# Kernel tuning notes

Measured on AMD Instinct MI355X. Metric: run time of the kernel, lower is better.

## Reference

```python
import jax, jax.numpy as jnp
import numpy as np

B, Z, OUT, NODES = 2048, 64, 512, 64
TRIPLES = 3 * (NODES - 1)  # (self, left, right) per real node
EPS_BN = 1e-5
EPS_TLN = 1e-5
SLOPE = 0.01  # LeakyReLU default


def setup_inputs() -> dict:
    key = jax.random.key(0)
    ks = jax.random.split(key, 12)
    def n(k, shape, s=0.05):
        return jax.random.normal(k, shape, jnp.float32) * s
    inp = {
        "trees": jax.random.normal(ks[0], (B, Z), jnp.float32),
        "indexes": jax.random.randint(ks[1], (B, TRIPLES, 1), 0, NODES),
        # MLP: Linear(Z,64) -> BN -> Linear(64,256) -> BN -> Linear(256,1024) -> BN -> Linear(1024,4096) -> BN
        "w1": n(ks[2], (64, Z)),      "b1": jnp.zeros((64,), jnp.float32),
        "g1": jnp.ones((64,), jnp.float32),   "be1": jnp.zeros((64,), jnp.float32),
        "w2": n(ks[3], (256, 64)),    "b2": jnp.zeros((256,), jnp.float32),
        "g2": jnp.ones((256,), jnp.float32),  "be2": jnp.zeros((256,), jnp.float32),
        "w3": n(ks[4], (1024, 256)),  "b3": jnp.zeros((1024,), jnp.float32),
        "g3": jnp.ones((1024,), jnp.float32), "be3": jnp.zeros((1024,), jnp.float32),
        "w4": n(ks[5], (4096, 1024)), "b4": jnp.zeros((4096,), jnp.float32),
        "g4": jnp.ones((4096,), jnp.float32), "be4": jnp.zeros((4096,), jnp.float32),
        # BinaryTreeConv weights: Conv1d(in,out,kernel=3,stride=3) -> (out,in,3)
        "cw1": n(ks[6], (128, 64, 3)),  "cb1": jnp.zeros((128,), jnp.float32),
        "cw2": n(ks[7], (256, 128, 3)), "cb2": jnp.zeros((256,), jnp.float32),
        "cw3": n(ks[8], (OUT, 256, 3)), "cb3": jnp.zeros((OUT,), jnp.float32),
    }
    return inp


def _bn(x, g, b):
    # BatchNorm1d in training mode: batch statistics, biased variance
    m = jnp.mean(x, axis=0)
    v = jnp.var(x, axis=0)
    return g * (x - m) * jax.lax.rsqrt(v + EPS_BN) + b


def _lrelu(x):
    return jnp.where(x > 0, x, SLOPE * x)


def _tree_conv(x, idx, w, b):
    # x: (B, C, N); idx: (B, 3M) node indices; w: (O, C, 3)
    Bn, C, _ = x.shape
    expanded = jnp.take_along_axis(x, idx[:, None, :], axis=2)  # (B, C, 3M) gather
    expanded = expanded.reshape(Bn, C, -1, 3)                    # (B, C, M, 3)
    out = jnp.einsum('bcmk,ock->bom', expanded, w) + b[None, :, None]
    zero = jnp.zeros((Bn, w.shape[0], 1), x.dtype)               # re-attach null-node slot
    return jnp.concatenate([zero, out], axis=2)                  # (B, O, M+1)


def _tree_norm(x):
    # TreeLayerNorm: normalize over (channels, nodes) per sample; torch.std is unbiased
    m = jnp.mean(x, axis=(1, 2), keepdims=True)
    s = jnp.std(x, axis=(1, 2), ddof=1, keepdims=True)
    return (x - m) / (s + EPS_TLN)


def reference(trees, indexes, w1, b1, g1, be1, w2, b2, g2, be2, w3, b3, g3, be3,
              w4, b4, g4, be4, cw1, cb1, cw2, cb2, cw3, cb3):
    idx = indexes[..., 0]  # (B, 3M)
    h = _lrelu(_bn(trees @ w1.T + b1, g1, be1))
    h = _lrelu(_bn(h @ w2.T + b2, g2, be2))
    h = _lrelu(_bn(h @ w3.T + b3, g3, be3))
    h = _lrelu(_bn(h @ w4.T + b4, g4, be4))
    x = h.reshape(h.shape[0], 64, 64)  # (B, C=64, N=64)
    x = _lrelu(_tree_norm(_tree_conv(x, idx, cw1, cb1)))
    x = _lrelu(_tree_norm(_tree_conv(x, idx, cw2, cb2)))
    x = _lrelu(_tree_norm(_tree_conv(x, idx, cw3, cb3)))
    return x  # (B, OUT, 64)
```

## Files before the change

kernel.cpp:

```cpp
#include <hip/hip_runtime.h>

typedef unsigned short u16;
typedef unsigned int   u32;
typedef __attribute__((ext_vector_type(8))) short short8;
typedef __attribute__((ext_vector_type(4))) float f32x4;
typedef __attribute__((ext_vector_type(4))) u16  u16x4;

#define DI __device__ __forceinline__

DI float b2f(u16 v){ return __builtin_bit_cast(float, (u32)v << 16); }
DI u16 f2b(float f){ u32 u = __builtin_bit_cast(u32, f); return (u16)((u + 0x7fffu + ((u >> 16) & 1u)) >> 16); }
DI float lrelu(float v){ return v > 0.f ? v : 0.01f * v; }

__global__ __launch_bounds__(256)
void cvt_bf16(const float* __restrict__ in, u16* __restrict__ out, int n4)
{
  int i = blockIdx.x*256 + threadIdx.x;
  if (i >= n4) return;
  float4 v = ((const float4*)in)[i];
  u16x4 o; o[0]=f2b(v.x); o[1]=f2b(v.y); o[2]=f2b(v.z); o[3]=f2b(v.w);
  *(u16x4*)(out + (size_t)i*4) = o;
}

template<int BM, int BN, int WROWS, int WCOLS, int RT, int CT>
__global__ __launch_bounds__(WROWS*WCOLS*64)
void gemm_nt(const u16* __restrict__ A, const u16* __restrict__ W,
             float* __restrict__ Y, int M, int N, int K)
{
  constexpr int NT  = WROWS*WCOLS*64;
  constexpr int ALD = (BM*4)/NT;
  constexpr int BLD = (BN*4)/NT;
  __shared__ __align__(16) u16 As[BM*32];
  __shared__ __align__(16) u16 Bs[BN*32];
  const int tid  = threadIdx.x;
  const int wave = tid >> 6, lane = tid & 63;
  const int wr = wave / WCOLS, wc = wave % WCOLS;
  const int lrow = lane & 15, kg = lane >> 4;
  const int m0 = blockIdx.x * BM, n0 = blockIdx.y * BN;
  f32x4 acc[RT][CT] = {};
  for (int k0 = 0; k0 < K; k0 += 32) {
    uint4 av[ALD], bv[BLD];
#pragma unroll
    for (int i = 0; i < ALD; i++){ int x = tid + i*NT; av[i] = *(const uint4*)(A + (size_t)(m0 + (x>>2))*K + k0 + (x&3)*8); }
#pragma unroll
    for (int i = 0; i < BLD; i++){ int x = tid + i*NT; bv[i] = *(const uint4*)(W + (size_t)(n0 + (x>>2))*K + k0 + (x&3)*8); }
    __syncthreads();
#pragma unroll
    for (int i = 0; i < ALD; i++){ *(uint4*)(As + (tid + i*NT)*8) = av[i]; }
#pragma unroll
    for (int i = 0; i < BLD; i++){ *(uint4*)(Bs + (tid + i*NT)*8) = bv[i]; }
    __syncthreads();
    short8 af[RT], bfr[CT];
#pragma unroll
    for (int r = 0; r < RT; r++) af[r]  = *(const short8*)(As + ((wr*RT + r)*16 + lrow)*32 + kg*8);
#pragma unroll
    for (int c = 0; c < CT; c++) bfr[c] = *(const short8*)(Bs + ((wc*CT + c)*16 + lrow)*32 + kg*8);
#pragma unroll
    for (int r = 0; r < RT; r++)
#pragma unroll
      for (int c = 0; c < CT; c++)
        acc[r][c] = __builtin_amdgcn_mfma_f32_16x16x32_bf16(af[r], bfr[c], acc[r][c], 0, 0, 0);
  }
#pragma unroll
  for (int r = 0; r < RT; r++)
#pragma unroll
    for (int c = 0; c < CT; c++)
#pragma unroll
      for (int i = 0; i < 4; i++){
        int m = m0 + (wr*RT + r)*16 + kg*4 + i;
        int n = n0 + (wc*CT + c)*16 + lrow;
        Y[(size_t)m*N + n] = acc[r][c][i];
      }
}

__global__ __launch_bounds__(256)
void bn_partial(const float* __restrict__ Y, float* __restrict__ part, int N, int rowsPer)
{
  const int tx = threadIdx.x & 63, ty = threadIdx.x >> 6;
  const int n  = blockIdx.x*64 + tx;
  const int m0 = blockIdx.y * rowsPer;
  float s = 0.f, s2 = 0.f;
  for (int m = m0 + ty; m < m0 + rowsPer; m += 4){ float v = Y[(size_t)m*N + n]; s += v; s2 += v*v; }
  __shared__ float ls[4][64], ls2[4][64];
  ls[ty][tx] = s; ls2[ty][tx] = s2;
  __syncthreads();
  if (ty == 0){
    s  = ls[0][tx]+ls[1][tx]+ls[2][tx]+ls[3][tx];
    s2 = ls2[0][tx]+ls2[1][tx]+ls2[2][tx]+ls2[3][tx];
    part[(size_t)(blockIdx.y*2+0)*N + n] = s;
    part[(size_t)(blockIdx.y*2+1)*N + n] = s2;
  }
}

__global__ __launch_bounds__(256)
void bn_finalize(const float* __restrict__ part, const float* __restrict__ g,
                 const float* __restrict__ be, float* __restrict__ ss, int N, int M, int split)
{
  int n = blockIdx.x*256 + threadIdx.x;
  if (n >= N) return;
  float s = 0.f, s2 = 0.f;
  for (int i = 0; i < split; i++){ s += part[(size_t)(i*2+0)*N + n]; s2 += part[(size_t)(i*2+1)*N + n]; }
  float inv  = 1.f / (float)M;
  float mean = s * inv;
  float var  = fmaxf(s2*inv - mean*mean, 0.f);
  float sc   = g[n] * rsqrtf(var + 1e-5f);
  ss[n]     = sc;
  ss[N + n] = be[n] - mean*sc;
}

__global__ __launch_bounds__(256)
void bn_apply(const float* __restrict__ Y, const float* __restrict__ ss,
              u16* __restrict__ H, int total4, int N)
{
  int i = blockIdx.x*256 + threadIdx.x;
  if (i >= total4) return;
  float4 v = ((const float4*)Y)[i];
  int nb = (i*4) & (N-1);
  u16x4 o;
  o[0] = f2b(lrelu(v.x*ss[nb+0] + ss[N+nb+0]));
  o[1] = f2b(lrelu(v.y*ss[nb+1] + ss[N+nb+1]));
  o[2] = f2b(lrelu(v.z*ss[nb+2] + ss[N+nb+2]));
  o[3] = f2b(lrelu(v.w*ss[nb+3] + ss[N+nb+3]));
  *(u16x4*)(H + (size_t)i*4) = o;
}

__global__ __launch_bounds__(256)
void bn_apply4_t(const float* __restrict__ Y, const float* __restrict__ ss, u16* __restrict__ Xt)
{
  const int b = blockIdx.x, tid = threadIdx.x;
  __shared__ u16 t[64*65];
  for (int j = tid; j < 4096; j += 256){
    float v = Y[(size_t)b*4096 + j];
    v = lrelu(v*ss[j] + ss[4096 + j]);
    int c = j >> 6, n = j & 63;
    t[c*65 + n] = f2b(v);
  }
  __syncthreads();
  for (int e = tid; e < 4096; e += 256){
    int n = e >> 6, c = e & 63;
    Xt[(size_t)b*4096 + n*64 + c] = t[c*65 + n];
  }
}

__global__ __launch_bounds__(256)
void repack_w_frag(const float* __restrict__ w, u16* __restrict__ wr, int O, int C, int lgC)
{
  int e = blockIdx.x*256 + threadIdx.x;
  int R = 3*C;
  if (e >= O*R) return;
  int NK   = R >> 5;
  int j    = e & 7;
  int lane = (e >> 3) & 63;
  int blk  = e >> 9;
  int tr   = blk / NK, kb = blk - tr*NK;
  int row  = tr*16 + (lane & 15);
  int kcol = kb*32 + (lane >> 4)*8 + j;
  int k = kcol >> lgC; int c = kcol & (C-1);
  wr[e] = f2b(w[(size_t)row*R + c*3 + k]);
}

template<int C, int O, int WAVES, int MINW, bool PIPE, bool LAST>
__global__ __launch_bounds__(WAVES*64, MINW)
void conv_norm(const u16* __restrict__ Xin, const u16* __restrict__ Wr,
               const float* __restrict__ cb, const int* __restrict__ gidx,
               u16* __restrict__ Xout, float* __restrict__ Outf)
{
  constexpr int R    = 3*C;
  constexpr int NK   = R/32;
  constexpr int CSI  = C + 8;
  constexpr int RT   = O/(WAVES*16);
  constexpr int NT   = WAVES*64;
  constexpr int LGC  = (C==64)?6:((C==128)?7:8);
  constexpr int LG32 = LGC - 5;
  __shared__ __align__(16) u16 xs[65*CSI];
  __shared__ int idxs[192];
  __shared__ float red[2*WAVES];
  const int b = blockIdx.x, tid = threadIdx.x;
  const int wave = tid >> 6, lane = tid & 63;
  const int lrow = lane & 15, kg = lane >> 4;

  const u16* xg = Xin + (size_t)b*64*C;
  for (int e = tid; e < 64*(C/8); e += NT){
    int row = e/(C/8), t = e%(C/8);
    *(uint4*)(xs + row*CSI + t*8) = *(const uint4*)(xg + row*C + t*8);
  }
  for (int e = tid; e < C/8; e += NT){ uint4 z = {0,0,0,0}; *(uint4*)(xs + 64*CSI + e*8) = z; }
  if (tid < 189){ int v = gidx[b*189 + tid]; idxs[tid] = v & 63; }
  __syncthreads();

  int jr0[4], jr1[4], jr2[4];
#pragma unroll
  for (int ct = 0; ct < 4; ct++){
    int n = ct*16 + lrow;
    jr0[ct] = (n == 0) ? 64 : idxs[3*(n-1) + 0];
    jr1[ct] = (n == 0) ? 64 : idxs[3*(n-1) + 1];
    jr2[ct] = (n == 0) ? 64 : idxs[3*(n-1) + 2];
  }

  const u16* wbase = Wr + ((size_t)wave*NK << 9) + lane*8;

  auto loadA = [&](short8* af, int kb32){
#pragma unroll
    for (int r = 0; r < RT; r++)
      af[r] = *(const short8*)(wbase + (((size_t)(WAVES*r)*NK + kb32) << 9));
  };
  auto loadB = [&](short8* bfr, int kb32){
    const int k  = kb32 >> LG32;
    const int c0 = ((kb32*32) & (C-1)) + kg*8;
#pragma unroll
    for (int ct = 0; ct < 4; ct++){
      int row = (k == 0) ? jr0[ct] : ((k == 1) ? jr1[ct] : jr2[ct]);
      bfr[ct] = *(const short8*)(xs + row*CSI + c0);
    }
  };

  f32x4 acc[RT][4] = {};
  auto domfma = [&](short8* af, short8* bfr){
    __builtin_amdgcn_s_setprio(1);
#pragma unroll
    for (int r = 0; r < RT; r++)
#pragma unroll
      for (int ct = 0; ct < 4; ct++)
        acc[r][ct] = __builtin_amdgcn_mfma_f32_16x16x32_bf16(af[r], bfr[ct], acc[r][ct], 0, 0, 0);
    __builtin_amdgcn_s_setprio(0);
  };

  if constexpr (PIPE) {
    short8 afA[RT], bfA[4], afB[RT], bfB[4];
    loadA(afA, 0); loadB(bfA, 0);
    for (int kb32 = 0; kb32 < NK; kb32 += 2){
      loadA(afB, kb32+1); loadB(bfB, kb32+1);
      domfma(afA, bfA);
      if (kb32 + 2 < NK){ loadA(afA, kb32+2); loadB(bfA, kb32+2); }
      domfma(afB, bfB);
    }
  } else {
    for (int kb32 = 0; kb32 < NK; kb32++){
      short8 af[RT], bfr[4];
      loadA(af, kb32); loadB(bfr, kb32);
      domfma(af, bfr);
    }
  }

  float s = 0.f, s2 = 0.f;
#pragma unroll
  for (int r = 0; r < RT; r++)
#pragma unroll
    for (int i = 0; i < 4; i++){
      int o = (wave + WAVES*r)*16 + kg*4 + i;
      float bias = cb[o];
#pragma unroll
      for (int ct = 0; ct < 4; ct++){
        int n = ct*16 + lrow;
        float v = acc[r][ct][i];
        if (n != 0) v += bias;
        acc[r][ct][i] = v;
        s += v; s2 += v*v;
      }
    }
#pragma unroll
  for (int off = 32; off > 0; off >>= 1){ s += __shfl_down(s, off); s2 += __shfl_down(s2, off); }
  if (lane == 0){ red[wave] = s; red[WAVES + wave] = s2; }
  __syncthreads();
  if (tid == 0){
    float S = 0.f, S2 = 0.f;
    for (int w = 0; w < WAVES; w++){ S += red[w]; S2 += red[WAVES + w]; }
    const float NV = (float)(O*64);
    float mean = S / NV;
    float var  = fmaxf(S2/NV - mean*mean, 0.f) * (NV/(NV-1.f));
    float sc   = 1.f / (sqrtf(var) + 1e-5f);
    red[0] = mean; red[1] = sc;
  }
  __syncthreads();
  const float mean = red[0], sc = red[1];

  if constexpr (LAST) {
#pragma unroll
    for (int r = 0; r < RT; r++)
#pragma unroll
      for (int ct = 0; ct < 4; ct++)
#pragma unroll
        for (int i = 0; i < 4; i++){
          int o = (wave + WAVES*r)*16 + kg*4 + i;
          int n = ct*16 + lrow;
          Outf[(size_t)b*(O*64) + o*64 + n] = lrelu((acc[r][ct][i] - mean)*sc);
        }
  } else {
#pragma unroll
    for (int r = 0; r < RT; r++)
#pragma unroll
      for (int ct = 0; ct < 4; ct++){
        int o0 = (wave + WAVES*r)*16 + kg*4;
        int n  = ct*16 + lrow;
        u16x4 pk;
#pragma unroll
        for (int i = 0; i < 4; i++) pk[i] = f2b(lrelu((acc[r][ct][i] - mean)*sc));
        *(u16x4*)(Xout + (size_t)b*64*O + (size_t)n*O + o0) = pk;
      }
  }
}

extern "C" void kernel_launch(void* const* d_in, const int* in_sizes, int n_in,
                              void* d_out, int out_size, void* d_ws, size_t ws_size,
                              hipStream_t stream)
{
  const float* trees = (const float*)d_in[0];
  const int*   gidx  = (const int*)d_in[1];
  const float* w1 = (const float*)d_in[2];
  const float* g1 = (const float*)d_in[4];  const float* be1 = (const float*)d_in[5];
  const float* w2 = (const float*)d_in[6];
  const float* g2 = (const float*)d_in[8];  const float* be2 = (const float*)d_in[9];
  const float* w3 = (const float*)d_in[10];
  const float* g3 = (const float*)d_in[12]; const float* be3 = (const float*)d_in[13];
  const float* w4 = (const float*)d_in[14];
  const float* g4 = (const float*)d_in[16]; const float* be4 = (const float*)d_in[17];
  const float* cw1 = (const float*)d_in[18]; const float* cb1 = (const float*)d_in[19];
  const float* cw2 = (const float*)d_in[20]; const float* cb2 = (const float*)d_in[21];
  const float* cw3 = (const float*)d_in[22]; const float* cb3 = (const float*)d_in[23];

  char* ws = (char*)d_ws;
  size_t off = 0;
  auto alloc = [&](size_t bytes)->char*{ char* p = ws + off; off += (bytes + 255) & ~(size_t)255; return p; };
  u16*   Wr1  = (u16*)  alloc(128*192*2);
  u16*   Wr2  = (u16*)  alloc(256*384*2);
  u16*   Wr3  = (u16*)  alloc(512*768*2);
  float* part = (float*)alloc(16*4096*4);
  float* ss1  = (float*)alloc(2*64*4);
  float* ss2  = (float*)alloc(2*256*4);
  float* ss3  = (float*)alloc(2*1024*4);
  float* ss4  = (float*)alloc(2*4096*4);
  u16*   Xc3  = (u16*)  alloc((size_t)2048*64*256*2);

  float* outF = (float*)d_out;
  u16*   ob   = (u16*)d_out;
  float* Y    = (float*)ob;
  u16*   H1   = ob + 16777216;
  u16*   H2   = ob + 16908288;
  u16*   H3   = ob + 17432576;
  u16*   Tb   = ob + 19529728;
  u16*   Wb1  = ob + 19660800;
  u16*   Wb2  = ob + 19664896;
  u16*   Wb3  = ob + 19681280;
  u16*   Wb4  = ob + 19943424;
  u16*   Xt1  = ob + 25165824;
  u16*   Xc2  = ob + 33554432;

  cvt_bf16<<<(131072/4+255)/256, 256, 0, stream>>>(trees, Tb, 131072/4);
  cvt_bf16<<<(4096/4+255)/256,   256, 0, stream>>>(w1, Wb1, 4096/4);
  cvt_bf16<<<(16384/4+255)/256,  256, 0, stream>>>(w2, Wb2, 16384/4);
  cvt_bf16<<<(262144/4+255)/256, 256, 0, stream>>>(w3, Wb3, 262144/4);
  cvt_bf16<<<(4194304/4+255)/256,256, 0, stream>>>(w4, Wb4, 4194304/4);

  repack_w_frag<<<(128*192+255)/256, 256, 0, stream>>>(cw1, Wr1, 128, 64, 6);
  repack_w_frag<<<(256*384+255)/256, 256, 0, stream>>>(cw2, Wr2, 256, 128, 7);
  repack_w_frag<<<(512*768+255)/256, 256, 0, stream>>>(cw3, Wr3, 512, 256, 8);

  gemm_nt<64,64,4,1,1,4><<<dim3(32,1), 256, 0, stream>>>(Tb, Wb1, Y, 2048, 64, 64);
  bn_partial<<<dim3(1,8), 256, 0, stream>>>(Y, part, 64, 256);
  bn_finalize<<<1, 256, 0, stream>>>(part, g1, be1, ss1, 64, 2048, 8);
  bn_apply<<<(2048*64/4+255)/256, 256, 0, stream>>>(Y, ss1, H1, 2048*64/4, 64);
  gemm_nt<64,64,4,1,1,4><<<dim3(32,4), 256, 0, stream>>>(H1, Wb2, Y, 2048, 256, 64);
  bn_partial<<<dim3(4,8), 256, 0, stream>>>(Y, part, 256, 256);
  bn_finalize<<<1, 256, 0, stream>>>(part, g2, be2, ss2, 256, 2048, 8);
  bn_apply<<<(2048*256/4+255)/256, 256, 0, stream>>>(Y, ss2, H2, 2048*256/4, 256);
  gemm_nt<64,64,4,1,1,4><<<dim3(32,16), 256, 0, stream>>>(H2, Wb3, Y, 2048, 1024, 256);
  bn_partial<<<dim3(16,8), 256, 0, stream>>>(Y, part, 1024, 256);
  bn_finalize<<<4, 256, 0, stream>>>(part, g3, be3, ss3, 1024, 2048, 8);
  bn_apply<<<(2048*1024/4+255)/256, 256, 0, stream>>>(Y, ss3, H3, 2048*1024/4, 1024);
  gemm_nt<128,128,2,2,4,4><<<dim3(16,32), 256, 0, stream>>>(H3, Wb4, Y, 2048, 4096, 1024);
  bn_partial<<<dim3(64,8), 256, 0, stream>>>(Y, part, 4096, 256);
  bn_finalize<<<16, 256, 0, stream>>>(part, g4, be4, ss4, 4096, 2048, 8);
  bn_apply4_t<<<2048, 256, 0, stream>>>(Y, ss4, Xt1);

  conv_norm< 64,128,8,4,true ,false><<<2048, 512, 0, stream>>>(Xt1, Wr1, cb1, gidx, Xc2, nullptr);
  conv_norm<128,256,8,4,true ,false><<<2048, 512, 0, stream>>>(Xc2, Wr2, cb2, gidx, Xc3, nullptr);
  conv_norm<256,512,8,4,false,true ><<<2048, 512, 0, stream>>>(Xc3, Wr3, cb3, gidx, nullptr, outF);
}
```

Measured before the change: 429.7 us.

## Fuse BN statistics into GEMM epilogue and BN apply into next GEMM's A-load

Column sums and sums of squares are now computed in the GEMM epilogue and written as per-block partials, which removes the separate bn_partial pass over Y. The normalize, LeakyReLU and bf16 conversion of the previous layer move into the next GEMM's A-tile load, which removes bn_apply and the bf16 input conversion. The cost is that the GEMM reads fp32 activations (twice the bytes of bf16) and repeats the scale/shift work for every N-block that reads the same rows. Two fp32 Y buffers now alternate between layers.

New measurement: 360.1 us. -16.2%, faster.

```diff
diff --git a/kernel.cpp b/kernel.cpp
--- a/kernel.cpp
+++ b/kernel.cpp
@@ -22,16 +22,19 @@
   *(u16x4*)(out + (size_t)i*4) = o;
 }
 
-template<int BM, int BN, int WROWS, int WCOLS, int RT, int CT>
+template<int BM, int BN, int WROWS, int WCOLS, int RT, int CT, bool APPLY>
 __global__ __launch_bounds__(WROWS*WCOLS*64)
-void gemm_nt(const u16* __restrict__ A, const u16* __restrict__ W,
-             float* __restrict__ Y, int M, int N, int K)
+void gemm_bn(const float* __restrict__ A, const u16* __restrict__ W,
+             const float* __restrict__ ssA,
+             float* __restrict__ Y, float* __restrict__ part,
+             int M, int N, int K)
 {
   constexpr int NT  = WROWS*WCOLS*64;
   constexpr int ALD = (BM*4)/NT;
   constexpr int BLD = (BN*4)/NT;
   __shared__ __align__(16) u16 As[BM*32];
   __shared__ __align__(16) u16 Bs[BN*32];
+  __shared__ float colS[WROWS][BN], colS2[WROWS][BN];
   const int tid  = threadIdx.x;
   const int wave = tid >> 6, lane = tid & 63;
   const int wr = wave / WCOLS, wc = wave % WCOLS;
@@ -41,7 +44,25 @@
   for (int k0 = 0; k0 < K; k0 += 32) {
     uint4 av[ALD], bv[BLD];
 #pragma unroll
-    for (int i = 0; i < ALD; i++){ int x = tid + i*NT; av[i] = *(const uint4*)(A + (size_t)(m0 + (x>>2))*K + k0 + (x&3)*8); }
+    for (int i = 0; i < ALD; i++){
+      int x = tid + i*NT; int kc = k0 + (x&3)*8;
+      const float* ap = A + (size_t)(m0 + (x>>2))*K + kc;
+      float4 y0 = *(const float4*)ap, y1 = *(const float4*)(ap + 4);
+      float v[8] = {y0.x,y0.y,y0.z,y0.w,y1.x,y1.y,y1.z,y1.w};
+      if constexpr (APPLY){
+        float4 c0 = *(const float4*)(ssA + kc),     c1 = *(const float4*)(ssA + kc + 4);
+        float4 h0 = *(const float4*)(ssA + K + kc), h1 = *(const float4*)(ssA + K + kc + 4);
+        v[0]=lrelu(v[0]*c0.x+h0.x); v[1]=lrelu(v[1]*c0.y+h0.y);
+        v[2]=lrelu(v[2]*c0.z+h0.z); v[3]=lrelu(v[3]*c0.w+h0.w);
+        v[4]=lrelu(v[4]*c1.x+h1.x); v[5]=lrelu(v[5]*c1.y+h1.y);
+        v[6]=lrelu(v[6]*c1.z+h1.z); v[7]=lrelu(v[7]*c1.w+h1.w);
+      }
+      u32 w0 = (u32)f2b(v[0]) | ((u32)f2b(v[1])<<16);
+      u32 w1 = (u32)f2b(v[2]) | ((u32)f2b(v[3])<<16);
+      u32 w2 = (u32)f2b(v[4]) | ((u32)f2b(v[5])<<16);
+      u32 w3 = (u32)f2b(v[6]) | ((u32)f2b(v[7])<<16);
+      av[i] = (uint4){w0,w1,w2,w3};
+    }
 #pragma unroll
     for (int i = 0; i < BLD; i++){ int x = tid + i*NT; bv[i] = *(const uint4*)(W + (size_t)(n0 + (x>>2))*K + k0 + (x&3)*8); }
     __syncthreads();
@@ -71,24 +92,24 @@
         int n = n0 + (wc*CT + c)*16 + lrow;
         Y[(size_t)m*N + n] = acc[r][c][i];
       }
-}
-
-__global__ __launch_bounds__(256)
-void bn_partial(const float* __restrict__ Y, float* __restrict__ part, int N, int rowsPer)
-{
-  const int tx = threadIdx.x & 63, ty = threadIdx.x >> 6;
-  const int n  = blockIdx.x*64 + tx;
-  const int m0 = blockIdx.y * rowsPer;
-  float s = 0.f, s2 = 0.f;
-  for (int m = m0 + ty; m < m0 + rowsPer; m += 4){ float v = Y[(size_t)m*N + n]; s += v; s2 += v*v; }
-  __shared__ float ls[4][64], ls2[4][64];
-  ls[ty][tx] = s; ls2[ty][tx] = s2;
-  __syncthreads();
-  if (ty == 0){
-    s  = ls[0][tx]+ls[1][tx]+ls[2][tx]+ls[3][tx];
-    s2 = ls2[0][tx]+ls2[1][tx]+ls2[2][tx]+ls2[3][tx];
-    part[(size_t)(blockIdx.y*2+0)*N + n] = s;
-    part[(size_t)(blockIdx.y*2+1)*N + n] = s2;
+#pragma unroll
+  for (int c = 0; c < CT; c++){
+    float s = 0.f, s2 = 0.f;
+#pragma unroll
+    for (int r = 0; r < RT; r++)
+#pragma unroll
+      for (int i = 0; i < 4; i++){ float v = acc[r][c][i]; s += v; s2 += v*v; }
+    s  += __shfl_xor(s, 16);  s  += __shfl_xor(s, 32);
+    s2 += __shfl_xor(s2, 16); s2 += __shfl_xor(s2, 32);
+    if (kg == 0){ colS[wr][(wc*CT + c)*16 + lrow] = s; colS2[wr][(wc*CT + c)*16 + lrow] = s2; }
+  }
+  __syncthreads();
+  if (tid < BN){
+    float S = 0.f, S2 = 0.f;
+#pragma unroll
+    for (int w = 0; w < WROWS; w++){ S += colS[w][tid]; S2 += colS2[w][tid]; }
+    part[(size_t)(blockIdx.x*2+0)*N + n0 + tid] = S;
+    part[(size_t)(blockIdx.x*2+1)*N + n0 + tid] = S2;
   }
 }
 
@@ -106,22 +127,6 @@
   float sc   = g[n] * rsqrtf(var + 1e-5f);
   ss[n]     = sc;
   ss[N + n] = be[n] - mean*sc;
-}
-
-__global__ __launch_bounds__(256)
-void bn_apply(const float* __restrict__ Y, const float* __restrict__ ss,
-              u16* __restrict__ H, int total4, int N)
-{
-  int i = blockIdx.x*256 + threadIdx.x;
-  if (i >= total4) return;
-  float4 v = ((const float4*)Y)[i];
-  int nb = (i*4) & (N-1);
-  u16x4 o;
-  o[0] = f2b(lrelu(v.x*ss[nb+0] + ss[N+nb+0]));
-  o[1] = f2b(lrelu(v.y*ss[nb+1] + ss[N+nb+1]));
-  o[2] = f2b(lrelu(v.z*ss[nb+2] + ss[N+nb+2]));
-  o[3] = f2b(lrelu(v.w*ss[nb+3] + ss[N+nb+3]));
-  *(u16x4*)(H + (size_t)i*4) = o;
 }
 
 __global__ __launch_bounds__(256)
@@ -324,28 +329,24 @@
   u16*   Wr1  = (u16*)  alloc(128*192*2);
   u16*   Wr2  = (u16*)  alloc(256*384*2);
   u16*   Wr3  = (u16*)  alloc(512*768*2);
-  float* part = (float*)alloc(16*4096*4);
+  float* part = (float*)alloc(64*4096*4);
   float* ss1  = (float*)alloc(2*64*4);
   float* ss2  = (float*)alloc(2*256*4);
   float* ss3  = (float*)alloc(2*1024*4);
   float* ss4  = (float*)alloc(2*4096*4);
   u16*   Xc3  = (u16*)  alloc((size_t)2048*64*256*2);
 
+  u16*   ob   = (u16*)d_out;
   float* outF = (float*)d_out;
-  u16*   ob   = (u16*)d_out;
-  float* Y    = (float*)ob;
-  u16*   H1   = ob + 16777216;
-  u16*   H2   = ob + 16908288;
-  u16*   H3   = ob + 17432576;
-  u16*   Tb   = ob + 19529728;
+  float* Ya   = (float*)ob;
   u16*   Wb1  = ob + 19660800;
   u16*   Wb2  = ob + 19664896;
   u16*   Wb3  = ob + 19681280;
   u16*   Wb4  = ob + 19943424;
   u16*   Xt1  = ob + 25165824;
   u16*   Xc2  = ob + 33554432;
-
-  cvt_bf16<<<(131072/4+255)/256, 256, 0, stream>>>(trees, Tb, 131072/4);
+  float* Yb   = (float*)(ob + 50331648);
+
   cvt_bf16<<<(4096/4+255)/256,   256, 0, stream>>>(w1, Wb1, 4096/4);
   cvt_bf16<<<(16384/4+255)/256,  256, 0, stream>>>(w2, Wb2, 16384/4);
   cvt_bf16<<<(262144/4+255)/256, 256, 0, stream>>>(w3, Wb3, 262144/4);
@@ -355,22 +356,15 @@
   repack_w_frag<<<(256*384+255)/256, 256, 0, stream>>>(cw2, Wr2, 256, 128, 7);
   repack_w_frag<<<(512*768+255)/256, 256, 0, stream>>>(cw3, Wr3, 512, 256, 8);
 
-  gemm_nt<64,64,4,1,1,4><<<dim3(32,1), 256, 0, stream>>>(Tb, Wb1, Y, 2048, 64, 64);
-  bn_partial<<<dim3(1,8), 256, 0, stream>>>(Y, part, 64, 256);
-  bn_finalize<<<1, 256, 0, stream>>>(part, g1, be1, ss1, 64, 2048, 8);
-  bn_apply<<<(2048*64/4+255)/256, 256, 0, stream>>>(Y, ss1, H1, 2048*64/4, 64);
-  gemm_nt<64,64,4,1,1,4><<<dim3(32,4), 256, 0, stream>>>(H1, Wb2, Y, 2048, 256, 64);
-  bn_partial<<<dim3(4,8), 256, 0, stream>>>(Y, part, 256, 256);
-  bn_finalize<<<1, 256, 0, stream>>>(part, g2, be2, ss2, 256, 2048, 8);
-  bn_apply<<<(2048*256/4+255)/256, 256, 0, stream>>>(Y, ss2, H2, 2048*256/4, 256);
-  gemm_nt<64,64,4,1,1,4><<<dim3(32,16), 256, 0, stream>>>(H2, Wb3, Y, 2048, 1024, 256);
-  bn_partial<<<dim3(16,8), 256, 0, stream>>>(Y, part, 1024, 256);
-  bn_finalize<<<4, 256, 0, stream>>>(part, g3, be3, ss3, 1024, 2048, 8);
-  bn_apply<<<(2048*1024/4+255)/256, 256, 0, stream>>>(Y, ss3, H3, 2048*1024/4, 1024);
-  gemm_nt<128,128,2,2,4,4><<<dim3(16,32), 256, 0, stream>>>(H3, Wb4, Y, 2048, 4096, 1024);
-  bn_partial<<<dim3(64,8), 256, 0, stream>>>(Y, part, 4096, 256);
-  bn_finalize<<<16, 256, 0, stream>>>(part, g4, be4, ss4, 4096, 2048, 8);
-  bn_apply4_t<<<2048, 256, 0, stream>>>(Y, ss4, Xt1);
+  gemm_bn<64,64,4,1,1,4,false><<<dim3(32,1), 256, 0, stream>>>(trees, Wb1, nullptr, Ya, part, 2048, 64, 64);
+  bn_finalize<<<1, 256, 0, stream>>>(part, g1, be1, ss1, 64, 2048, 32);
+  gemm_bn<64,64,4,1,1,4,true ><<<dim3(32,4), 256, 0, stream>>>(Ya, Wb2, ss1, Yb, part, 2048, 256, 64);
+  bn_finalize<<<1, 256, 0, stream>>>(part, g2, be2, ss2, 256, 2048, 32);
+  gemm_bn<64,64,4,1,1,4,true ><<<dim3(32,16), 256, 0, stream>>>(Yb, Wb3, ss2, Ya, part, 2048, 1024, 256);
+  bn_finalize<<<4, 256, 0, stream>>>(part, g3, be3, ss3, 1024, 2048, 32);
+  gemm_bn<128,128,2,2,4,4,true><<<dim3(16,32), 256, 0, stream>>>(Ya, Wb4, ss3, Yb, part, 2048, 4096, 1024);
+  bn_finalize<<<16, 256, 0, stream>>>(part, g4, be4, ss4, 4096, 2048, 16);
+  bn_apply4_t<<<2048, 256, 0, stream>>>(Yb, ss4, Xt1);
 
   conv_norm< 64,128,8,4,true ,false><<<2048, 512, 0, stream>>>(Xt1, Wr1, cb1, gidx, Xc2, nullptr);
   conv_norm<128,256,8,4,true ,false><<<2048, 512, 0, stream>>>(Xc2, Wr2, cb2, gidx, Xc3, nullptr);
```
